# Optimization experiments

Measured on AMD Instinct MI355X. Metric: run time of the kernel, lower is better.

Reference implementation:

```python
import jax, jax.numpy as jnp
import numpy as np

KS = 3          # kernel_size
M = 6           # num_bases
TEM = 6         # tem_size = (KS//2)*num_bases
BN_EPS = 1e-3   # keras BatchNormalization default epsilon


def _conv(x, w):
    # x: NCHW, w: OIHW, stride 1, SAME padding (module uses padding='same')
    return jax.lax.conv_general_dilated(x, w, (1, 1), 'SAME',
                                        dimension_numbers=('NCHW', 'OIHW', 'NCHW'))


def _bn(x, gamma, beta, mean, var):
    # inference-mode batchnorm over channel dim (NCHW)
    s = gamma * jax.lax.rsqrt(var + BN_EPS)
    return x * s[None, :, None, None] + (beta - mean * s)[None, :, None, None]


def _unfold(x):
    # im2col: N,C,H,W -> N,C,KS*KS,H,W with SAME padding, stride 1
    N, C, H, W = x.shape
    xp = jnp.pad(x, ((0, 0), (0, 0), (1, 1), (1, 1)))
    taps = [xp[:, :, i:i + H, j:j + W] for i in range(KS) for j in range(KS)]
    return jnp.stack(taps, axis=2)


def setup_inputs() -> dict:
    key = jax.random.key(0)
    ks = jax.random.split(key, 16)
    N, C, O, H, W = 16, 128, 128, 64, 64
    inter, bsz = 64, M * TEM  # 64, 36
    x = jax.random.normal(ks[0], (N, C, H, W), jnp.float32)
    w1 = jax.random.normal(ks[1], (inter, C, 3, 3), jnp.float32) * (1.0 / np.sqrt(C * 9))
    gamma1 = jnp.ones((inter,), jnp.float32)
    beta1 = jnp.zeros((inter,), jnp.float32)
    mean1 = jax.random.normal(ks[2], (inter,), jnp.float32) * 0.1
    var1 = jax.random.uniform(ks[3], (inter,), jnp.float32, 0.5, 1.5)
    w2 = jax.random.normal(ks[4], (bsz, inter, 3, 3), jnp.float32) * (1.0 / np.sqrt(inter * 9))
    gamma2 = jnp.ones((bsz,), jnp.float32)
    beta2 = jnp.zeros((bsz,), jnp.float32)
    mean2 = jax.random.normal(ks[5], (bsz,), jnp.float32) * 0.1
    var2 = jax.random.uniform(ks[6], (bsz,), jnp.float32, 0.5, 1.5)
    # Fixed Fourier-Bessel-style basis [TEM, KS*KS], normalized as in calculate_FB_bases
    rng = np.random.RandomState(0)
    psi = rng.normal(size=(KS * KS, TEM)).astype(np.float32)
    c = np.sqrt((psi ** 2).sum(0).mean())
    fb_bases = jnp.asarray((psi / c).T)  # [TEM, 9]
    coef = jax.random.normal(ks[7], (O, C * M), jnp.float32) * np.sqrt(2.0 / (C * M))
    bias = jnp.zeros((O,), jnp.float32)
    return {'x': x, 'w1': w1, 'gamma1': gamma1, 'beta1': beta1, 'mean1': mean1,
            'var1': var1, 'w2': w2, 'gamma2': gamma2, 'beta2': beta2,
            'mean2': mean2, 'var2': var2, 'fb_bases': fb_bases, 'coef': coef,
            'bias': bias}


def reference(x, w1, gamma1, beta1, mean1, var1, w2, gamma2, beta2, mean2, var2,
              fb_bases, coef, bias):
    N, C, H, W = x.shape
    # bases_net: conv3x3 -> BN -> tanh -> conv3x3 -> BN -> tanh
    h = jnp.tanh(_bn(_conv(x, w1), gamma1, beta1, mean1, var1))
    b = jnp.tanh(_bn(_conv(h, w2), gamma2, beta2, mean2, var2))   # N,36,H,W
    bcoef = b.reshape(N, M, TEM, H, W)
    # combine predicted coefficients with fixed FB bases -> per-pixel filters
    bases = jnp.einsum('bmkhw,kl->bmlhw', bcoef, fb_bases)        # N,M,9,H,W
    xu = _unfold(x)                                               # N,C,9,H,W
    # per-pixel gather-multiply-reduce over the 9 taps
    bo = jnp.einsum('bmlhw,bclhw->bcmhw', bases, xu)              # N,C,M,H,W
    bo = bo.reshape(N, C * M, H, W)
    # 1x1 conv with coef + bias
    out = jnp.einsum('bkhw,ok->bohw', bo, coef) + bias[None, :, None, None]
    return out
```

## Files before the change

### kernel.cpp

```cpp
#include <hip/hip_runtime.h>
#include <hip/hip_bf16.h>

using bf16 = __hip_bfloat16;
typedef __attribute__((ext_vector_type(8))) short bf16x8;
typedef __attribute__((ext_vector_type(4))) float f32x4;
typedef __attribute__((ext_vector_type(2))) float f32x2;

#define BN_EPS 1e-3f

#define OFF_W1M   16u
#define OFF_B1F   36880u
#define OFF_W2M   36944u
#define OFF_B2F   50768u
#define OFF_FBF   50804u
#define OFF_CFM   50860u
#define OFF_BIASF 100012u
#define OFF_BB    100144u

__device__ __forceinline__ int dtype_flag(const void* g1) {
    return ((const unsigned*)g1)[0] != 0x3F800000u;
}

__device__ __forceinline__ float b2f(bf16 v) { return __bfloat162float(v); }
__device__ __forceinline__ unsigned short f2b(float f) {
    union { bf16 h; unsigned short u; } cv;
    cv.h = __float2bfloat16(f);
    return cv.u;
}
__device__ __forceinline__ unsigned packbf(float a, float b) {
    return (unsigned)f2b(a) | ((unsigned)f2b(b) << 16);
}
__device__ __forceinline__ float ldin(const void* p, long long i, int f) {
    return f ? b2f(((const bf16*)p)[i]) : ((const float*)p)[i];
}
__device__ __forceinline__ float lo_f(unsigned u) { return __uint_as_float(u << 16); }
__device__ __forceinline__ float hi_f(unsigned u) { return __uint_as_float(u & 0xFFFF0000u); }
__device__ __forceinline__ void ld8f(const void* p, long long i, int f, float* o) {
    if (f) {
        uint4 v = *(const uint4*)((const unsigned short*)p + i);
        o[0] = lo_f(v.x); o[1] = hi_f(v.x); o[2] = lo_f(v.y); o[3] = hi_f(v.y);
        o[4] = lo_f(v.z); o[5] = hi_f(v.z); o[6] = lo_f(v.w); o[7] = hi_f(v.w);
    } else {
        const float* q = (const float*)p + i;
        float4 a = *(const float4*)q, b = *(const float4*)(q + 4);
        o[0] = a.x; o[1] = a.y; o[2] = a.z; o[3] = a.w;
        o[4] = b.x; o[5] = b.y; o[6] = b.z; o[7] = b.w;
    }
}
__device__ __forceinline__ bf16x8 lds_frag(const unsigned short* p) {
    uint2 lo = *(const uint2*)p;
    uint2 hi = *(const uint2*)(p + 4);
    union { unsigned u[4]; bf16x8 v; } r;
    r.u[0] = lo.x; r.u[1] = lo.y; r.u[2] = hi.x; r.u[3] = hi.y;
    return r.v;
}

__global__ __launch_bounds__(256) void prep_kernel(
    const void* __restrict__ w1, const void* __restrict__ g1, const void* __restrict__ be1,
    const void* __restrict__ mu1, const void* __restrict__ va1,
    const void* __restrict__ w2, const void* __restrict__ g2, const void* __restrict__ be2,
    const void* __restrict__ mu2, const void* __restrict__ va2,
    const void* __restrict__ fb, const void* __restrict__ coef, const void* __restrict__ bias,
    float* __restrict__ ws)
{
    const int f = dtype_flag(g1);
    int j = blockIdx.x * 256 + threadIdx.x;
    if (j < 73728) {
        int tap = j >> 13, r = j & 8191;
        int ntile = r >> 11, r2 = r & 2047;
        int ks = r2 >> 9, r3 = r2 & 511;
        int lane = r3 >> 3, jj = r3 & 7;
        int oc = ntile * 16 + (lane & 15);
        int ic = ks * 32 + (lane >> 4) * 8 + jj;
        float s = ldin(g1, oc, f) * rsqrtf(ldin(va1, oc, f) + BN_EPS);
        ((unsigned short*)(ws + OFF_W1M))[j] = f2b(ldin(w1, (oc * 128 + ic) * 9 + tap, f) * s);
        return;
    }
    j -= 73728;
    if (j < 64) {
        float s = ldin(g1, j, f) * rsqrtf(ldin(va1, j, f) + BN_EPS);
        ws[OFF_B1F + j] = ldin(be1, j, f) - ldin(mu1, j, f) * s;
        return;
    }
    j -= 64;
    if (j < 27648) {
        int tap = j / 3072, r = j - tap * 3072;
        int ntile = r >> 10, r2 = r & 1023;
        int ks = r2 >> 9, r3 = r2 & 511;
        int lane = r3 >> 3, jj = r3 & 7;
        int oc = ntile * 16 + (lane & 15);
        int ic = ks * 32 + (lane >> 4) * 8 + jj;
        float v = 0.f;
        if (oc < 36) {
            float s = ldin(g2, oc, f) * rsqrtf(ldin(va2, oc, f) + BN_EPS);
            v = ldin(w2, (oc * 64 + ic) * 9 + tap, f) * s;
        }
        ((unsigned short*)(ws + OFF_W2M))[j] = f2b(v);
        return;
    }
    j -= 27648;
    if (j < 36) {
        float s = ldin(g2, j, f) * rsqrtf(ldin(va2, j, f) + BN_EPS);
        ws[OFF_B2F + j] = ldin(be2, j, f) - ldin(mu2, j, f) * s;
        return;
    }
    j -= 36;
    if (j < 54) { ws[OFF_FBF + j] = ldin(fb, j, f); return; }
    j -= 54;
    if (j < 98304) {
        int chunk = j / 12288, r = j - chunk * 12288;
        int ks = r >> 12, r2 = r & 4095;
        int ntile = r2 >> 9, r3 = r2 & 511;
        int lane = r3 >> 3, jj = r3 & 7;
        int o = ntile * 16 + (lane & 15);
        int k = chunk * 96 + ks * 32 + (lane >> 4) * 8 + jj;
        ((unsigned short*)(ws + OFF_CFM))[j] = f2b(ldin(coef, o * 768 + k, f));
        return;
    }
    j -= 98304;
    if (j < 128) { ws[OFF_BIASF + j] = ldin(bias, j, f); return; }
}

__global__ __launch_bounds__(512, 8) void conv1_mfma(
    const void* __restrict__ x, const void* __restrict__ g1, const float* __restrict__ ws,
    unsigned short* __restrict__ hbuf)
{
    __shared__ unsigned short sA[3][66][132];
    unsigned* sAu = (unsigned*)sA;
    const unsigned short* w1m = (const unsigned short*)(ws + OFF_W1M);
    const int f = dtype_flag(g1);
    const int t = threadIdx.x;
    const int n = blockIdx.x >> 6, h = blockIdx.x & 63;

    for (int e = t; e < 396; e += 512) {
        int dy = e / 132, q = e - dy * 132;
        int wrow = (q >= 66) ? 65 : 0;
        int cu = (q >= 66) ? q - 66 : q;
        sAu[(dy * 66 + wrow) * 66 + cu] = 0u;
    }
    {
        const long long xb = (long long)n * 128 * 4096;
        for (int u = t; u < 1536; u += 512) {
            int dy = u >> 9, rem = u & 511, icp = rem >> 3, w8 = rem & 7;
            int hh = h + dy - 1;
            float va[8], vb[8];
            if (hh >= 0 && hh < 64) {
                long long base = xb + (long long)(icp * 2) * 4096 + hh * 64 + w8 * 8;
                ld8f(x, base, f, va);
                ld8f(x, base + 4096, f, vb);
            } else {
#pragma unroll
                for (int i = 0; i < 8; ++i) { va[i] = 0.f; vb[i] = 0.f; }
            }
            const int wb_ = w8 * 8 + 1;
#pragma unroll
            for (int i = 0; i < 8; ++i)
                sAu[(dy * 66 + wb_ + i) * 66 + icp] = packbf(va[i], vb[i]);
        }
    }
    __syncthreads();

    const int wv = t >> 6, lane = t & 63;
    const int fr = lane & 15, quad = lane >> 4;
    const int mh = (wv & 3) * 16;
    const int nh = (wv >> 2) * 32;
    const int ntb = nh >> 4;

    f32x4 acc[2];
#pragma unroll
    for (int j = 0; j < 2; ++j) acc[j] = (f32x4){0.f, 0.f, 0.f, 0.f};

#pragma unroll
    for (int tap = 0; tap < 9; ++tap) {
        const int dy = tap / 3, dx = tap - dy * 3;
#pragma unroll
        for (int ks = 0; ks < 4; ++ks) {
            const int kof = ks * 32 + quad * 8;
            bf16x8 a = lds_frag(&sA[dy][mh + fr + dx][kof]);
            bf16x8 b0 = *(const bf16x8*)(w1m + (((tap * 4 + ntb) * 4 + ks) * 64 + lane) * 8);
            bf16x8 b1 = *(const bf16x8*)(w1m + (((tap * 4 + ntb + 1) * 4 + ks) * 64 + lane) * 8);
            acc[0] = __builtin_amdgcn_mfma_f32_16x16x32_bf16(a, b0, acc[0], 0, 0, 0);
            acc[1] = __builtin_amdgcn_mfma_f32_16x16x32_bf16(a, b1, acc[1], 0, 0, 0);
        }
    }

#pragma unroll
    for (int nt = 0; nt < 2; ++nt) {
        int oc = nh + nt * 16 + fr;
        int m0 = mh + quad * 4;
        float bv = ws[OFF_B1F + oc];
        f32x4 v = acc[nt];
        union { unsigned short us[4]; uint2 u; } pk;
#pragma unroll
        for (int i = 0; i < 4; ++i) pk.us[i] = f2b(tanhf(v[i] + bv));
        *(uint2*)(hbuf + (size_t)(n * 64 + oc) * 4096 + h * 64 + m0) = pk.u;
    }
}

__global__ __launch_bounds__(512, 8) void conv2_mfma(
    const float* __restrict__ ws, const unsigned short* __restrict__ hbuf,
    float* __restrict__ bbout)
{
    __shared__ unsigned short sA[3][66][68];
    unsigned* sAu = (unsigned*)sA;
    const unsigned short* w2m = (const unsigned short*)(ws + OFF_W2M);
    const int t = threadIdx.x;
    const int n = blockIdx.x >> 6, h = blockIdx.x & 63;

    for (int e = t; e < 204; e += 512) {
        int dy = e / 68, q = e - dy * 68;
        int wrow = (q >= 34) ? 65 : 0;
        int cu = (q >= 34) ? q - 34 : q;
        sAu[(dy * 66 + wrow) * 34 + cu] = 0u;
    }
    {
        const unsigned short* hn = hbuf + (size_t)n * 64 * 4096;
        for (int u = t; u < 768; u += 512) {
            int dy = u >> 8, rem = u & 255, icp = rem >> 3, w8 = rem & 7;
            int hh = h + dy - 1;
            uint4 a = make_uint4(0u, 0u, 0u, 0u), b = a;
            if (hh >= 0 && hh < 64) {
                const unsigned short* p = hn + (size_t)(icp * 2) * 4096 + hh * 64 + w8 * 8;
                a = *(const uint4*)p;
                b = *(const uint4*)(p + 4096);
            }
            const int wb_ = w8 * 8 + 1;
            unsigned au[4] = {a.x, a.y, a.z, a.w}, bu[4] = {b.x, b.y, b.z, b.w};
#pragma unroll
            for (int jj = 0; jj < 4; ++jj) {
                unsigned lo = (au[jj] & 0xFFFFu) | (bu[jj] << 16);
                unsigned hi = (au[jj] >> 16) | (bu[jj] & 0xFFFF0000u);
                sAu[(dy * 66 + wb_ + 2 * jj) * 34 + icp] = lo;
                sAu[(dy * 66 + wb_ + 2 * jj + 1) * 34 + icp] = hi;
            }
        }
    }
    __syncthreads();

    const int wv = t >> 6, lane = t & 63;
    const int fr = lane & 15, quad = lane >> 4;
    const int m0 = (wv & 3) * 16;
    const int ngrp = wv >> 2;

    f32x4 acc[2];
#pragma unroll
    for (int i = 0; i < 2; ++i) acc[i] = (f32x4){0.f, 0.f, 0.f, 0.f};

#pragma unroll
    for (int tap = 0; tap < 9; ++tap) {
        const int dy = tap / 3, dx = tap - dy * 3;
#pragma unroll
        for (int ks = 0; ks < 2; ++ks) {
            const int kof = ks * 32 + quad * 8;
            bf16x8 a = lds_frag(&sA[dy][m0 + fr + dx][kof]);
            if (ngrp == 0) {
                bf16x8 b0 = *(const bf16x8*)(w2m + (((tap * 3 + 0) * 2 + ks) * 64 + lane) * 8);
                bf16x8 b1 = *(const bf16x8*)(w2m + (((tap * 3 + 1) * 2 + ks) * 64 + lane) * 8);
                acc[0] = __builtin_amdgcn_mfma_f32_16x16x32_bf16(a, b0, acc[0], 0, 0, 0);
                acc[1] = __builtin_amdgcn_mfma_f32_16x16x32_bf16(a, b1, acc[1], 0, 0, 0);
            } else {
                bf16x8 b2 = *(const bf16x8*)(w2m + (((tap * 3 + 2) * 2 + ks) * 64 + lane) * 8);
                acc[0] = __builtin_amdgcn_mfma_f32_16x16x32_bf16(a, b2, acc[0], 0, 0, 0);
            }
        }
    }

    const int pbase = (n << 12) + h * 64 + m0 + quad * 4;
    if (ngrp == 0) {
#pragma unroll
        for (int nt = 0; nt < 2; ++nt) {
            int oc = nt * 16 + fr;
            float bv = ws[OFF_B2F + oc];
            f32x4 v = acc[nt];
#pragma unroll
            for (int reg = 0; reg < 4; ++reg)
                bbout[(size_t)(pbase + reg) * 36 + oc] = tanhf(v[reg] + bv);
        }
    } else {
        int oc = 32 + fr;
        if (oc < 36) {
            float bv = ws[OFF_B2F + oc];
            f32x4 v = acc[0];
#pragma unroll
            for (int reg = 0; reg < 4; ++reg)
                bbout[(size_t)(pbase + reg) * 36 + oc] = tanhf(v[reg] + bv);
        }
    }
}

__global__ __launch_bounds__(512, 8) void fuse_kernel(
    const void* __restrict__ x, const void* __restrict__ g1, const float* __restrict__ ws,
    void* __restrict__ outv)
{
    __shared__ float sbT[64][60];
    __shared__ __align__(16) unsigned short slbo[64][104];
    __shared__ __align__(16) unsigned short sX[3][66][22];
    unsigned* sXu = (unsigned*)sX;

    const float* bbp = ws + OFF_BB;
    const float* fbf = ws + OFF_FBF;
    const unsigned short* cfm = (const unsigned short*)(ws + OFF_CFM);
    const int f = dtype_flag(g1);

    const int t = threadIdx.x;
    const int p0 = blockIdx.x * 64;
    const int n = p0 >> 12;
    const int h = (p0 >> 6) & 63;

    const long long xbase = (long long)n * 128 * 4096;
    const int sw = t & 63, sg = t >> 6;

    float rv0[3], rv1[3];
#pragma unroll
    for (int dy = 0; dy < 3; ++dy) {
        int hh = h + dy - 1;
        float v0 = 0.f, v1 = 0.f;
        if (hh >= 0 && hh < 64) {
            long long base = xbase + (long long)(sg * 2) * 4096 + hh * 64 + sw;
            v0 = ldin(x, base, f);
            v1 = ldin(x, base + 4096, f);
        }
        rv0[dy] = v0; rv1[dy] = v1;
    }

    for (int task = t; task < 64 * 54; task += 512) {
        int p = task & 63, j = task >> 6;
        int m = j / 9, l = j - m * 9;
        const float* br = bbp + (size_t)(p0 + p) * 36 + m * 6;
        float s = 0.f;
#pragma unroll
        for (int k = 0; k < 6; ++k) s += br[k] * fbf[k * 9 + l];
        sbT[p][l * 6 + m] = s;
    }
    if (t < 66) {
        int dy = t / 22, q = t - dy * 22;
        int wrow = (q >= 11) ? 65 : 0;
        int cu = (q >= 11) ? q - 11 : q;
        sXu[(dy * 66 + wrow) * 11 + cu] = 0u;
    }

    const int pp = t >> 3, cl = t & 7;
    const int wv = t >> 6, lane = t & 63;
    const int fr = lane & 15, quad = lane >> 4;
    const int m0w = (wv & 3) * 16;
    const int nh = (wv >> 2) * 64;
    const int ntb = nh >> 4;

    f32x4 acc[4];
#pragma unroll
    for (int nt = 0; nt < 4; ++nt) acc[nt] = (f32x4){0.f, 0.f, 0.f, 0.f};

    __syncthreads();

#pragma unroll
    for (int chunk = 0; chunk < 8; ++chunk) {
#pragma unroll
        for (int dy = 0; dy < 3; ++dy)
            sXu[(dy * 66 + sw + 1) * 11 + sg] = packbf(rv0[dy], rv1[dy]);
        __syncthreads();
        if (chunk < 7) {
            const int c0n = (chunk + 1) * 16;
#pragma unroll
            for (int dy = 0; dy < 3; ++dy) {
                int hh = h + dy - 1;
                float v0 = 0.f, v1 = 0.f;
                if (hh >= 0 && hh < 64) {
                    long long base = xbase + (long long)(c0n + sg * 2) * 4096 + hh * 64 + sw;
                    v0 = ldin(x, base, f);
                    v1 = ldin(x, base + 4096, f);
                }
                rv0[dy] = v0; rv1[dy] = v1;
            }
        }
        {
            f32x2 xv[9];
#pragma unroll
            for (int dy = 0; dy < 3; ++dy)
#pragma unroll
                for (int dx = 0; dx < 3; ++dx) {
                    unsigned d = sXu[(dy * 66 + pp + dx) * 11 + cl];
                    xv[dy * 3 + dx] = (f32x2){lo_f(d), hi_f(d)};
                }
            f32x2 sm2[6];
#pragma unroll
            for (int m = 0; m < 6; ++m) sm2[m] = (f32x2){0.f, 0.f};
            const float* sp = &sbT[pp][0];
#pragma unroll
            for (int jv = 0; jv < 13; ++jv) {
                f32x4 s4 = *(const f32x4*)(sp + jv * 4);
#pragma unroll
                for (int e = 0; e < 4; ++e) {
                    const int j = jv * 4 + e;
                    const int l = j / 6, m = j - l * 6;
                    sm2[m] += xv[l] * s4[e];
                }
            }
            {
                f32x2 s2 = *(const f32x2*)(sp + 52);
                sm2[4] += xv[8] * s2[0];
                sm2[5] += xv[8] * s2[1];
            }
            unsigned* du = (unsigned*)slbo + pp * 52 + cl * 6;
            uint2 w0 = make_uint2(packbf(sm2[0][0], sm2[1][0]), packbf(sm2[2][0], sm2[3][0]));
            uint2 w1 = make_uint2(packbf(sm2[4][0], sm2[5][0]), packbf(sm2[0][1], sm2[1][1]));
            uint2 w2 = make_uint2(packbf(sm2[2][1], sm2[3][1]), packbf(sm2[4][1], sm2[5][1]));
            *(uint2*)&du[0] = w0;
            *(uint2*)&du[2] = w1;
            *(uint2*)&du[4] = w2;
        }
        __syncthreads();
#pragma unroll
        for (int ks = 0; ks < 3; ++ks) {
            const int kof = ks * 32 + quad * 8;
            bf16x8 a = *(const bf16x8*)&slbo[m0w + fr][kof];
            const unsigned short* cb = cfm + ((chunk * 3 + ks) * 8 + ntb) * 512 + lane * 8;
            bf16x8 b0 = *(const bf16x8*)(cb);
            bf16x8 b1 = *(const bf16x8*)(cb + 512);
            bf16x8 b2 = *(const bf16x8*)(cb + 1024);
            bf16x8 b3 = *(const bf16x8*)(cb + 1536);
            acc[0] = __builtin_amdgcn_mfma_f32_16x16x32_bf16(a, b0, acc[0], 0, 0, 0);
            acc[1] = __builtin_amdgcn_mfma_f32_16x16x32_bf16(a, b1, acc[1], 0, 0, 0);
            acc[2] = __builtin_amdgcn_mfma_f32_16x16x32_bf16(a, b2, acc[2], 0, 0, 0);
            acc[3] = __builtin_amdgcn_mfma_f32_16x16x32_bf16(a, b3, acc[3], 0, 0, 0);
        }
    }

    const int mrow = m0w + quad * 4;
#pragma unroll
    for (int nt = 0; nt < 4; ++nt) {
        int o = nh + nt * 16 + fr;
        float bv = ws[OFF_BIASF + o];
        f32x4 v = acc[nt];
        size_t ofs = (size_t)(n * 128 + o) * 4096 + h * 64 + mrow;
        if (f) {
            union { unsigned short us[4]; uint2 u; } pk;
#pragma unroll
            for (int i = 0; i < 4; ++i) pk.us[i] = f2b(v[i] + bv);
            *(uint2*)((unsigned short*)outv + ofs) = pk.u;
        } else {
            float4 w4 = make_float4(v[0] + bv, v[1] + bv, v[2] + bv, v[3] + bv);
            *(float4*)((float*)outv + ofs) = w4;
        }
    }
}

extern "C" void kernel_launch(void* const* d_in, const int* in_sizes, int n_in,
                              void* d_out, int out_size, void* d_ws, size_t ws_size,
                              hipStream_t stream)
{
    float* ws = (float*)d_ws;
    unsigned short* hbuf = (unsigned short*)d_out;

    hipLaunchKernelGGL(prep_kernel, dim3(782), dim3(256), 0, stream,
                       d_in[1], d_in[2], d_in[3], d_in[4], d_in[5],
                       d_in[6], d_in[7], d_in[8], d_in[9], d_in[10],
                       d_in[11], d_in[12], d_in[13], ws);
    hipLaunchKernelGGL(conv1_mfma, dim3(1024), dim3(512), 0, stream, d_in[0], d_in[2], ws, hbuf);
    hipLaunchKernelGGL(conv2_mfma, dim3(1024), dim3(512), 0, stream, ws, hbuf, ws + OFF_BB);
    hipLaunchKernelGGL(fuse_kernel, dim3(1024), dim3(512), 0, stream, d_in[0], d_in[2], ws, d_out);
}
```

Baseline: 200.4 us.

## Compute two output rows per block in conv1/conv2 with channel-phased staging

Measured after the change: 199.4 us. No clear change (-0.5%).

```diff
diff --git a/kernel.cpp b/kernel.cpp
--- a/kernel.cpp
+++ b/kernel.cpp
@@ -125,27 +125,38 @@
     const void* __restrict__ x, const void* __restrict__ g1, const float* __restrict__ ws,
     unsigned short* __restrict__ hbuf)
 {
-    __shared__ unsigned short sA[3][66][132];
+    __shared__ unsigned short sA[4][66][68];
     unsigned* sAu = (unsigned*)sA;
     const unsigned short* w1m = (const unsigned short*)(ws + OFF_W1M);
     const int f = dtype_flag(g1);
     const int t = threadIdx.x;
-    const int n = blockIdx.x >> 6, h = blockIdx.x & 63;
-
-    for (int e = t; e < 396; e += 512) {
-        int dy = e / 132, q = e - dy * 132;
-        int wrow = (q >= 66) ? 65 : 0;
-        int cu = (q >= 66) ? q - 66 : q;
-        sAu[(dy * 66 + wrow) * 66 + cu] = 0u;
-    }
-    {
-        const long long xb = (long long)n * 128 * 4096;
-        for (int u = t; u < 1536; u += 512) {
-            int dy = u >> 9, rem = u & 511, icp = rem >> 3, w8 = rem & 7;
-            int hh = h + dy - 1;
+    const int n = blockIdx.x >> 5, h0 = (blockIdx.x & 31) * 2;
+
+    for (int e = t; e < 272; e += 512) {
+        int dy = e / 68, q = e - dy * 68;
+        int wrow = (q >= 34) ? 65 : 0;
+        int cu = (q >= 34) ? q - 34 : q;
+        sAu[(dy * 66 + wrow) * 34 + cu] = 0u;
+    }
+
+    const int wv = t >> 6, lane = t & 63;
+    const int fr = lane & 15, quad = lane >> 4;
+    const int lr = wv >> 2;
+    const int wcol = (wv & 3) * 16;
+
+    f32x4 acc[4];
+#pragma unroll
+    for (int i = 0; i < 4; ++i) acc[i] = (f32x4){0.f, 0.f, 0.f, 0.f};
+
+    const long long xb = (long long)n * 128 * 4096;
+#pragma unroll
+    for (int ph = 0; ph < 2; ++ph) {
+        for (int u = t; u < 1024; u += 512) {
+            int dy = u >> 8, rem = u & 255, icp = rem >> 3, w8 = rem & 7;
+            int hh = h0 + dy - 1;
             float va[8], vb[8];
             if (hh >= 0 && hh < 64) {
-                long long base = xb + (long long)(icp * 2) * 4096 + hh * 64 + w8 * 8;
+                long long base = xb + (long long)(ph * 64 + icp * 2) * 4096 + hh * 64 + w8 * 8;
                 ld8f(x, base, f, va);
                 ld8f(x, base + 4096, f, vb);
             } else {
@@ -155,45 +166,38 @@
             const int wb_ = w8 * 8 + 1;
 #pragma unroll
             for (int i = 0; i < 8; ++i)
-                sAu[(dy * 66 + wb_ + i) * 66 + icp] = packbf(va[i], vb[i]);
-        }
-    }
-    __syncthreads();
-
-    const int wv = t >> 6, lane = t & 63;
-    const int fr = lane & 15, quad = lane >> 4;
-    const int mh = (wv & 3) * 16;
-    const int nh = (wv >> 2) * 32;
-    const int ntb = nh >> 4;
-
-    f32x4 acc[2];
-#pragma unroll
-    for (int j = 0; j < 2; ++j) acc[j] = (f32x4){0.f, 0.f, 0.f, 0.f};
-
-#pragma unroll
-    for (int tap = 0; tap < 9; ++tap) {
-        const int dy = tap / 3, dx = tap - dy * 3;
-#pragma unroll
-        for (int ks = 0; ks < 4; ++ks) {
-            const int kof = ks * 32 + quad * 8;
-            bf16x8 a = lds_frag(&sA[dy][mh + fr + dx][kof]);
-            bf16x8 b0 = *(const bf16x8*)(w1m + (((tap * 4 + ntb) * 4 + ks) * 64 + lane) * 8);
-            bf16x8 b1 = *(const bf16x8*)(w1m + (((tap * 4 + ntb + 1) * 4 + ks) * 64 + lane) * 8);
-            acc[0] = __builtin_amdgcn_mfma_f32_16x16x32_bf16(a, b0, acc[0], 0, 0, 0);
-            acc[1] = __builtin_amdgcn_mfma_f32_16x16x32_bf16(a, b1, acc[1], 0, 0, 0);
-        }
-    }
-
-#pragma unroll
-    for (int nt = 0; nt < 2; ++nt) {
-        int oc = nh + nt * 16 + fr;
-        int m0 = mh + quad * 4;
+                sAu[(dy * 66 + wb_ + i) * 34 + icp] = packbf(va[i], vb[i]);
+        }
+        __syncthreads();
+#pragma unroll
+        for (int tap = 0; tap < 9; ++tap) {
+            const int tdy = tap / 3, dx = tap - tdy * 3;
+            const int dyr = lr + tdy;
+#pragma unroll
+            for (int ks = 0; ks < 2; ++ks) {
+                const int kof = ks * 32 + quad * 8;
+                const int kg = ph * 2 + ks;
+                bf16x8 a = lds_frag(&sA[dyr][wcol + fr + dx][kof]);
+#pragma unroll
+                for (int nt = 0; nt < 4; ++nt) {
+                    bf16x8 b = *(const bf16x8*)(w1m + (((tap * 4 + nt) * 4 + kg) * 64 + lane) * 8);
+                    acc[nt] = __builtin_amdgcn_mfma_f32_16x16x32_bf16(a, b, acc[nt], 0, 0, 0);
+                }
+            }
+        }
+        if (ph == 0) __syncthreads();
+    }
+
+    const int w0 = wcol + quad * 4;
+#pragma unroll
+    for (int nt = 0; nt < 4; ++nt) {
+        int oc = nt * 16 + fr;
         float bv = ws[OFF_B1F + oc];
         f32x4 v = acc[nt];
         union { unsigned short us[4]; uint2 u; } pk;
 #pragma unroll
         for (int i = 0; i < 4; ++i) pk.us[i] = f2b(tanhf(v[i] + bv));
-        *(uint2*)(hbuf + (size_t)(n * 64 + oc) * 4096 + h * 64 + m0) = pk.u;
+        *(uint2*)(hbuf + (size_t)(n * 64 + oc) * 4096 + (h0 + lr) * 64 + w0) = pk.u;
     }
 }
 
@@ -201,13 +205,13 @@
     const float* __restrict__ ws, const unsigned short* __restrict__ hbuf,
     float* __restrict__ bbout)
 {
-    __shared__ unsigned short sA[3][66][68];
+    __shared__ unsigned short sA[4][66][68];
     unsigned* sAu = (unsigned*)sA;
     const unsigned short* w2m = (const unsigned short*)(ws + OFF_W2M);
     const int t = threadIdx.x;
-    const int n = blockIdx.x >> 6, h = blockIdx.x & 63;
-
-    for (int e = t; e < 204; e += 512) {
+    const int n = blockIdx.x >> 5, h0 = (blockIdx.x & 31) * 2;
+
+    for (int e = t; e < 272; e += 512) {
         int dy = e / 68, q = e - dy * 68;
         int wrow = (q >= 34) ? 65 : 0;
         int cu = (q >= 34) ? q - 34 : q;
@@ -215,9 +219,9 @@
     }
     {
         const unsigned short* hn = hbuf + (size_t)n * 64 * 4096;
-        for (int u = t; u < 768; u += 512) {
+        for (int u = t; u < 1024; u += 512) {
             int dy = u >> 8, rem = u & 255, icp = rem >> 3, w8 = rem & 7;
-            int hh = h + dy - 1;
+            int hh = h0 + dy - 1;
             uint4 a = make_uint4(0u, 0u, 0u, 0u), b = a;
             if (hh >= 0 && hh < 64) {
                 const unsigned short* p = hn + (size_t)(icp * 2) * 4096 + hh * 64 + w8 * 8;
@@ -239,52 +243,46 @@
 
     const int wv = t >> 6, lane = t & 63;
     const int fr = lane & 15, quad = lane >> 4;
-    const int m0 = (wv & 3) * 16;
-    const int ngrp = wv >> 2;
-
-    f32x4 acc[2];
-#pragma unroll
-    for (int i = 0; i < 2; ++i) acc[i] = (f32x4){0.f, 0.f, 0.f, 0.f};
+    const int lr = wv >> 2;
+    const int wcol = (wv & 3) * 16;
+
+    f32x4 acc[3];
+#pragma unroll
+    for (int i = 0; i < 3; ++i) acc[i] = (f32x4){0.f, 0.f, 0.f, 0.f};
 
 #pragma unroll
     for (int tap = 0; tap < 9; ++tap) {
-        const int dy = tap / 3, dx = tap - dy * 3;
+        const int tdy = tap / 3, dx = tap - tdy * 3;
+        const int dyr = lr + tdy;
 #pragma unroll
         for (int ks = 0; ks < 2; ++ks) {
             const int kof = ks * 32 + quad * 8;
-            bf16x8 a = lds_frag(&sA[dy][m0 + fr + dx][kof]);
-            if (ngrp == 0) {
-                bf16x8 b0 = *(const bf16x8*)(w2m + (((tap * 3 + 0) * 2 + ks) * 64 + lane) * 8);
-                bf16x8 b1 = *(const bf16x8*)(w2m + (((tap * 3 + 1) * 2 + ks) * 64 + lane) * 8);
-                acc[0] = __builtin_amdgcn_mfma_f32_16x16x32_bf16(a, b0, acc[0], 0, 0, 0);
-                acc[1] = __builtin_amdgcn_mfma_f32_16x16x32_bf16(a, b1, acc[1], 0, 0, 0);
-            } else {
-                bf16x8 b2 = *(const bf16x8*)(w2m + (((tap * 3 + 2) * 2 + ks) * 64 + lane) * 8);
-                acc[0] = __builtin_amdgcn_mfma_f32_16x16x32_bf16(a, b2, acc[0], 0, 0, 0);
-            }
-        }
-    }
-
-    const int pbase = (n << 12) + h * 64 + m0 + quad * 4;
-    if (ngrp == 0) {
-#pragma unroll
-        for (int nt = 0; nt < 2; ++nt) {
-            int oc = nt * 16 + fr;
-            float bv = ws[OFF_B2F + oc];
-            f32x4 v = acc[nt];
-#pragma unroll
-            for (int reg = 0; reg < 4; ++reg)
-                bbout[(size_t)(pbase + reg) * 36 + oc] = tanhf(v[reg] + bv);
-        }
-    } else {
+            bf16x8 a = lds_frag(&sA[dyr][wcol + fr + dx][kof]);
+#pragma unroll
+            for (int nt = 0; nt < 3; ++nt) {
+                bf16x8 b = *(const bf16x8*)(w2m + (((tap * 3 + nt) * 2 + ks) * 64 + lane) * 8);
+                acc[nt] = __builtin_amdgcn_mfma_f32_16x16x32_bf16(a, b, acc[nt], 0, 0, 0);
+            }
+        }
+    }
+
+    const int pbase = (n << 12) + (h0 + lr) * 64 + wcol + quad * 4;
+#pragma unroll
+    for (int nt = 0; nt < 2; ++nt) {
+        int oc = nt * 16 + fr;
+        float bv = ws[OFF_B2F + oc];
+        f32x4 v = acc[nt];
+#pragma unroll
+        for (int reg = 0; reg < 4; ++reg)
+            bbout[(size_t)(pbase + reg) * 36 + oc] = tanhf(v[reg] + bv);
+    }
+    if (fr < 4) {
         int oc = 32 + fr;
-        if (oc < 36) {
-            float bv = ws[OFF_B2F + oc];
-            f32x4 v = acc[0];
-#pragma unroll
-            for (int reg = 0; reg < 4; ++reg)
-                bbout[(size_t)(pbase + reg) * 36 + oc] = tanhf(v[reg] + bv);
-        }
+        float bv = ws[OFF_B2F + oc];
+        f32x4 v = acc[2];
+#pragma unroll
+        for (int reg = 0; reg < 4; ++reg)
+            bbout[(size_t)(pbase + reg) * 36 + oc] = tanhf(v[reg] + bv);
     }
 }
 
@@ -455,7 +453,7 @@
                        d_in[1], d_in[2], d_in[3], d_in[4], d_in[5],
                        d_in[6], d_in[7], d_in[8], d_in[9], d_in[10],
                        d_in[11], d_in[12], d_in[13], ws);
-    hipLaunchKernelGGL(conv1_mfma, dim3(1024), dim3(512), 0, stream, d_in[0], d_in[2], ws, hbuf);
-    hipLaunchKernelGGL(conv2_mfma, dim3(1024), dim3(512), 0, stream, ws, hbuf, ws + OFF_BB);
+    hipLaunchKernelGGL(conv1_mfma, dim3(512), dim3(512), 0, stream, d_in[0], d_in[2], ws, hbuf);
+    hipLaunchKernelGGL(conv2_mfma, dim3(512), dim3(512), 0, stream, ws, hbuf, ws + OFF_BB);
     hipLaunchKernelGGL(fuse_kernel, dim3(1024), dim3(512), 0, stream, d_in[0], d_in[2], ws, d_out);
 }
```
